# Performance work log

Measured on AMD Instinct MI355X. Metric: run time of the kernel, lower is better.

The kernel has to match this reference:

```python
import jax, jax.numpy as jnp
import numpy as np

B, T, C, H = 16, 2048, 512, 64


def _skew(x):
    # x: (B, T1, T2) -> relative-position skew trick (Music Transformer)
    b, t1, t2 = x.shape
    x = jnp.pad(x, ((0, 0), (0, 0), (1, 0)))        # pad one column on the left
    x = x.reshape(b, t2 + 1, t1)                    # reinterpret layout
    x = x[:, 1:, :]                                 # drop first row
    return jnp.transpose(x, (0, 2, 1))              # (B, T1, T2)


def setup_inputs() -> dict:
    key = jax.random.key(0)
    ks = jax.random.split(key, 5)
    return {
        "x": jax.random.normal(ks[0], (B, T, C), dtype=jnp.float32),
        "Wq": jax.random.normal(ks[1], (C, H), dtype=jnp.float32) * 0.02,
        "Wk": jax.random.normal(ks[2], (C, H), dtype=jnp.float32) * 0.02,
        "Wv": jax.random.normal(ks[3], (C, H), dtype=jnp.float32) * 0.02,
        "Er": jax.random.normal(ks[4], (T, H), dtype=jnp.float32),
    }


def reference(x, Wq, Wk, Wv, Er):
    b, t, c = x.shape
    q = x @ Wq  # (B, T, H)
    k = x @ Wk
    v = x @ Wv
    scale = 1.0 / (k.shape[-1] ** 0.5)
    att = jnp.einsum("bth,bsh->bts", q, k) * scale  # (B, T, T)
    # relative position bias via skew trick
    rel_att = jnp.einsum("bth,rh->btr", q, Er[:t])  # (B, T, T)
    att = att + _skew(rel_att)
    # causal mask
    mask = jnp.tril(jnp.ones((t, t), dtype=bool))
    att = jnp.where(mask, att, -jnp.inf)
    att = jax.nn.softmax(att, axis=-1)
    # dropout is identity in eval mode
    out = att @ v  # (B, T, H)
    return out
```

## Files before the change

kernel.cpp:

```cpp
#include <hip/hip_runtime.h>
#include <hip/hip_bf16.h>

#define TT 2048
#define HB 64
#define NB 16

typedef __attribute__((ext_vector_type(8))) short short8;
typedef __attribute__((ext_vector_type(4))) float floatx4;

static __device__ __forceinline__ unsigned short f2bf(float f) {
  __hip_bfloat16 h = __float2bfloat16(f);
  return *reinterpret_cast<unsigned short*>(&h);
}
static __device__ __forceinline__ float bf2f(unsigned short u) {
  __hip_bfloat16 h = *reinterpret_cast<__hip_bfloat16*>(&u);
  return __bfloat162float(h);
}

__global__ __launch_bounds__(256) void prep_kernel(
    const float* __restrict__ Wq, const float* __restrict__ Wk,
    const float* __restrict__ Wv, const float* __restrict__ Er,
    unsigned short* __restrict__ Wt, unsigned short* __restrict__ Erb) {
  const int bx = blockIdx.x, tid = threadIdx.x;
  if (bx < 512) {
    int idx = bx * 256 + tid;
    Erb[idx] = f2bf(Er[idx]);
  } else {
    int n = bx - 512;
    const float* Ws[3] = {Wq, Wk, Wv};
#pragma unroll
    for (int m = 0; m < 3; m++)
      for (int k = tid; k < 512; k += 256)
        Wt[(size_t)(m * 64 + n) * 512 + k] = f2bf(Ws[m][(size_t)k * 64 + n]);
  }
}

__global__ __launch_bounds__(256) void proj_kernel(
    const float* __restrict__ x, const unsigned short* __restrict__ Wt,
    unsigned short* __restrict__ qb, unsigned short* __restrict__ kb,
    unsigned short* __restrict__ vT) {
  const int tid = threadIdx.x;
  const int w = tid >> 6, l = tid & 63, quad = l >> 4, lm = l & 15;
  const int m0 = blockIdx.x * 64;
  const int row_a = m0 + w * 16 + lm;

  floatx4 acc[12];
#pragma unroll
  for (int i = 0; i < 12; i++) acc[i] = (floatx4){0.f, 0.f, 0.f, 0.f};

  for (int kt = 0; kt < 512; kt += 64) {
    short8 af[2];
#pragma unroll
    for (int kc = 0; kc < 2; kc++) {
      const float* px = &x[(size_t)row_a * 512 + kt + kc * 32 + quad * 8];
      float4 f0 = *(const float4*)px;
      float4 f1 = *(const float4*)(px + 4);
      short8 s;
      s[0] = f2bf(f0.x); s[1] = f2bf(f0.y); s[2] = f2bf(f0.z); s[3] = f2bf(f0.w);
      s[4] = f2bf(f1.x); s[5] = f2bf(f1.y); s[6] = f2bf(f1.z); s[7] = f2bf(f1.w);
      af[kc] = s;
    }
#pragma unroll
    for (int nt = 0; nt < 12; nt++) {
      const unsigned short* pw =
          &Wt[(size_t)((nt >> 2) * 64 + (nt & 3) * 16 + lm) * 512 + kt + quad * 8];
      short8 b0 = *(const short8*)pw;
      short8 b1 = *(const short8*)(pw + 32);
      acc[nt] = __builtin_amdgcn_mfma_f32_16x16x32_bf16(af[0], b0, acc[nt], 0, 0, 0);
      acc[nt] = __builtin_amdgcn_mfma_f32_16x16x32_bf16(af[1], b1, acc[nt], 0, 0, 0);
    }
  }
  const int b = m0 >> 11;
#pragma unroll
  for (int nt = 0; nt < 12; nt++) {
    int col = (nt & 3) * 16 + lm;
#pragma unroll
    for (int rg = 0; rg < 4; rg++) {
      int row = m0 + w * 16 + quad * 4 + rg;
      unsigned short hv = f2bf(acc[nt][rg]);
      if (nt < 4) qb[(size_t)row * 64 + col] = hv;
      else if (nt < 8) kb[(size_t)row * 64 + col] = hv;
      else vT[(size_t)(b * 64 + col) * 2048 + (row & 2047)] = hv;
    }
  }
}

#define SLICE_B 11264

__global__ __launch_bounds__(256) void attn_kernel(
    const unsigned short* __restrict__ qb, const unsigned short* __restrict__ kb,
    const unsigned short* __restrict__ vT, const unsigned short* __restrict__ Erb,
    float* __restrict__ out, float* __restrict__ Op, float* __restrict__ mp,
    float* __restrict__ lp, int nsplit) {
  __shared__ __align__(16) char smem[4 * SLICE_B];

  const int tid = threadIdx.x;
  const int w = tid >> 6;
  if (w >= nsplit) return;
  const int lane = tid & 63;
  const int quad = lane >> 4, lm = lane & 15;

  float* Ds = (float*)(smem + w * SLICE_B);
  unsigned short* Ps = (unsigned short*)(smem + w * SLICE_B + 8448);
  float* dbv = (float*)(smem + w * SLICE_B + 8448 + 2560);

  const int xcd = blockIdx.x & 7;
  const int u = blockIdx.x >> 3;
  const int b = xcd + ((u & 1) << 3);
  const int it = 63 - (u >> 1);
  const int i0 = it * 32;
  const int s = w;

  const size_t qoff = (size_t)b * (2048 * 64);
  const unsigned short* qB = qb + qoff;
  const unsigned short* kB = kb + qoff;
  const unsigned short* vB = vT + qoff;

  short8 qf[2][2];
#pragma unroll
  for (int mt = 0; mt < 2; mt++)
#pragma unroll
    for (int kc = 0; kc < 2; kc++)
      qf[mt][kc] =
          *(const short8*)&qB[(size_t)(i0 + mt * 16 + lm) * 64 + kc * 32 + quad * 8];

  {
    short8 ebf[2];
#pragma unroll
    for (int kc = 0; kc < 2; kc++) {
      short8 z = (short8){0, 0, 0, 0, 0, 0, 0, 0};
      if (lm == 0)
        z = *(const short8*)&Erb[(size_t)2047 * 64 + kc * 32 + quad * 8];
      ebf[kc] = z;
    }
#pragma unroll
    for (int mt = 0; mt < 2; mt++) {
      floatx4 dacc = (floatx4){0.f, 0.f, 0.f, 0.f};
      dacc = __builtin_amdgcn_mfma_f32_16x16x32_bf16(qf[mt][0], ebf[0], dacc, 0, 0, 0);
      dacc = __builtin_amdgcn_mfma_f32_16x16x32_bf16(qf[mt][1], ebf[1], dacc, 0, 0, 0);
      if (lm == 0) {
#pragma unroll
        for (int rg = 0; rg < 4; rg++)
          dbv[mt * 16 + quad * 4 + rg] = dacc[rg];
      }
    }
  }
  __builtin_amdgcn_wave_barrier();

  floatx4 O[2][4];
#pragma unroll
  for (int mt = 0; mt < 2; mt++)
#pragma unroll
    for (int nt = 0; nt < 4; nt++) O[mt][nt] = (floatx4){0.f, 0.f, 0.f, 0.f};
  float m_st[2][4], l_st[2][4];
#pragma unroll
  for (int mt = 0; mt < 2; mt++)
#pragma unroll
    for (int rg = 0; rg < 4; rg++) { m_st[mt][rg] = -1e30f; l_st[mt][rg] = 0.f; }

  for (int jt = s; jt <= it; jt += nsplit) {
    const int j0 = jt * 32;
    const int d = i0 - j0;
    const int e0 = (d - 33 > 0) ? (d - 33) : 0;

    short8 kf[2][2], uf[2][2], ef[4][2], vf[4];
#pragma unroll
    for (int t = 0; t < 2; t++)
#pragma unroll
      for (int kc = 0; kc < 2; kc++)
        kf[t][kc] =
            *(const short8*)&kB[(size_t)(j0 + t * 16 + lm) * 64 + kc * 32 + quad * 8];
#pragma unroll
    for (int ct = 0; ct < 2; ct++)
#pragma unroll
      for (int kc = 0; kc < 2; kc++) {
        int ur = j0 + ct * 16 + lm + 1;
        if (ur > 2047) ur = 2047;
        uf[ct][kc] = *(const short8*)&qB[(size_t)ur * 64 + kc * 32 + quad * 8];
      }
#pragma unroll
    for (int et = 0; et < 4; et++)
#pragma unroll
      for (int kc = 0; kc < 2; kc++)
        ef[et][kc] = *(const short8*)&Erb[(size_t)(e0 + et * 16 + lm) * 64 +
                                          kc * 32 + quad * 8];
#pragma unroll
    for (int nt = 0; nt < 4; nt++)
      vf[nt] = *(const short8*)&vB[(size_t)(nt * 16 + lm) * 2048 + j0 + quad * 8];

    __builtin_amdgcn_wave_barrier();

#pragma unroll
    for (int ct = 0; ct < 2; ct++)
#pragma unroll
      for (int et = 0; et < 4; et++) {
        floatx4 dacc = (floatx4){0.f, 0.f, 0.f, 0.f};
        dacc = __builtin_amdgcn_mfma_f32_16x16x32_bf16(uf[ct][0], ef[et][0], dacc, 0, 0, 0);
        dacc = __builtin_amdgcn_mfma_f32_16x16x32_bf16(uf[ct][1], ef[et][1], dacc, 0, 0, 0);
#pragma unroll
        for (int rg = 0; rg < 4; rg++)
          Ds[(ct * 16 + quad * 4 + rg) * 66 + et * 16 + lm] = dacc[rg];
      }

    floatx4 S[2][2];
#pragma unroll
    for (int mt = 0; mt < 2; mt++)
#pragma unroll
      for (int t = 0; t < 2; t++) {
        floatx4 a = (floatx4){0.f, 0.f, 0.f, 0.f};
        a = __builtin_amdgcn_mfma_f32_16x16x32_bf16(qf[mt][0], kf[t][0], a, 0, 0, 0);
        a = __builtin_amdgcn_mfma_f32_16x16x32_bf16(qf[mt][1], kf[t][1], a, 0, 0, 0);
        S[mt][t] = a;
      }

    __builtin_amdgcn_wave_barrier();
    asm volatile("s_waitcnt lgkmcnt(0)" ::: "memory");
    __builtin_amdgcn_sched_barrier(0);

#pragma unroll
    for (int mt = 0; mt < 2; mt++)
#pragma unroll
      for (int rg = 0; rg < 4; rg++) {
        const int rloc = mt * 16 + quad * 4 + rg;
        const int i = i0 + rloc;
        float sv[2];
#pragma unroll
        for (int t = 0; t < 2; t++) {
          int j = j0 + t * 16 + lm;
          float raw = 0.125f * S[mt][t][rg];
          float val;
          if (j > i) val = -1e30f;
          else if (j == i) val = raw + dbv[rloc];
          else if (j == i - 1) val = raw;
          else val = raw + Ds[(t * 16 + lm) * 66 + (i - j - 2 - e0)];
          sv[t] = val;
        }
        float mx = fmaxf(sv[0], sv[1]);
        mx = fmaxf(mx, __shfl_xor(mx, 1));
        mx = fmaxf(mx, __shfl_xor(mx, 2));
        mx = fmaxf(mx, __shfl_xor(mx, 4));
        mx = fmaxf(mx, __shfl_xor(mx, 8));
        float m_new = fmaxf(m_st[mt][rg], mx);
        float alpha = __expf(m_st[mt][rg] - m_new);
        float p0 = __expf(sv[0] - m_new);
        float p1 = __expf(sv[1] - m_new);
        float ps = p0 + p1;
        ps += __shfl_xor(ps, 1);
        ps += __shfl_xor(ps, 2);
        ps += __shfl_xor(ps, 4);
        ps += __shfl_xor(ps, 8);
        l_st[mt][rg] = l_st[mt][rg] * alpha + ps;
        m_st[mt][rg] = m_new;
#pragma unroll
        for (int nt = 0; nt < 4; nt++) O[mt][nt][rg] *= alpha;
        Ps[rloc * 40 + lm] = f2bf(p0);
        Ps[rloc * 40 + 16 + lm] = f2bf(p1);
      }

    __builtin_amdgcn_wave_barrier();
    asm volatile("s_waitcnt lgkmcnt(0)" ::: "memory");
    __builtin_amdgcn_sched_barrier(0);

#pragma unroll
    for (int mt = 0; mt < 2; mt++) {
      short8 pa = *(const short8*)&Ps[(mt * 16 + lm) * 40 + quad * 8];
#pragma unroll
      for (int nt = 0; nt < 4; nt++)
        O[mt][nt] = __builtin_amdgcn_mfma_f32_16x16x32_bf16(pa, vf[nt], O[mt][nt], 0, 0, 0);
    }
  }

  if (nsplit == 1) {
#pragma unroll
    for (int mt = 0; mt < 2; mt++)
#pragma unroll
      for (int rg = 0; rg < 4; rg++) {
        float inv = 1.f / l_st[mt][rg];
        int row = i0 + mt * 16 + quad * 4 + rg;
#pragma unroll
        for (int nt = 0; nt < 4; nt++)
          out[qoff + (size_t)row * 64 + nt * 16 + lm] = O[mt][nt][rg] * inv;
      }
  } else {
    float* Ops = Op + (size_t)s * (NB * TT * HB);
#pragma unroll
    for (int mt = 0; mt < 2; mt++)
#pragma unroll
      for (int rg = 0; rg < 4; rg++) {
        int row = i0 + mt * 16 + quad * 4 + rg;
#pragma unroll
        for (int nt = 0; nt < 4; nt++)
          Ops[qoff + (size_t)row * 64 + nt * 16 + lm] = O[mt][nt][rg];
        if (lm == 0) {
          int grow = b * 2048 + row;
          mp[s * 32768 + grow] = m_st[mt][rg];
          lp[s * 32768 + grow] = l_st[mt][rg];
        }
      }
  }
}

__global__ __launch_bounds__(256) void combine_kernel(
    const float* __restrict__ Op, const float* __restrict__ mp,
    const float* __restrict__ lp, float* __restrict__ out, int nsplit) {
  int gid = blockIdx.x * 256 + threadIdx.x;
  int row = gid >> 4;
  float m = -1e30f;
  for (int s = 0; s < nsplit; s++) m = fmaxf(m, mp[s * 32768 + row]);
  float den = 0.f;
  float4 r = {0.f, 0.f, 0.f, 0.f};
  for (int s = 0; s < nsplit; s++) {
    float a = __expf(mp[s * 32768 + row] - m);
    den += a * lp[s * 32768 + row];
    float4 o = *(const float4*)&Op[(size_t)s * 2097152 + (size_t)gid * 4];
    r.x += a * o.x;
    r.y += a * o.y;
    r.z += a * o.z;
    r.w += a * o.w;
  }
  float inv = 1.f / den;
  r.x *= inv; r.y *= inv; r.z *= inv; r.w *= inv;
  *(float4*)&out[(size_t)gid * 4] = r;
}

extern "C" void kernel_launch(void* const* d_in, const int* in_sizes, int n_in,
                              void* d_out, int out_size, void* d_ws,
                              size_t ws_size, hipStream_t stream) {
  const float* x = (const float*)d_in[0];
  const float* Wq = (const float*)d_in[1];
  const float* Wk = (const float*)d_in[2];
  const float* Wv = (const float*)d_in[3];
  const float* Er = (const float*)d_in[4];
  float* out = (float*)d_out;

  unsigned short* qb = (unsigned short*)d_ws;
  unsigned short* kb = qb + 2097152;
  unsigned short* vT = kb + 2097152;
  unsigned short* Wt = vT + 2097152;
  unsigned short* Erb = Wt + 98304;
  const size_t base = 13041664ull;
  const size_t need4 = base + 4ull * 8650752ull;
  const size_t need2 = base + 2ull * 8650752ull;
  const int nsplit = (ws_size >= need4) ? 4 : (ws_size >= need2) ? 2 : 1;

  float* Op = (float*)(Erb + 131072);
  float* mp = Op + (size_t)nsplit * 2097152;
  float* lp = mp + (size_t)nsplit * 32768;

  prep_kernel<<<576, 256, 0, stream>>>(Wq, Wk, Wv, Er, Wt, Erb);
  proj_kernel<<<512, 256, 0, stream>>>(x, Wt, qb, kb, vT);
  attn_kernel<<<1024, 256, 0, stream>>>(qb, kb, vT, Erb, out, Op, mp, lp,
                                        nsplit);
  if (nsplit > 1)
    combine_kernel<<<2048, 256, 0, stream>>>(Op, mp, lp, out, nsplit);
}
```

Measured before the change: 253.6 us.

## Fuse split-KV combine into attention kernel, pair causal tiles, skip rescale

The separate combine kernel and its global partial buffers are replaced by an in-block merge of the four waves' partial softmax states through shared memory, with the output written directly. Each block now handles two query tiles (it and 63-it) to balance causal work across 512 blocks. The online softmax skips the max reduction and rescale when every new score stays within a margin of the running max, and the row sum is reduced only once at the end. This removes the global round trip of partial outputs and one kernel launch, at the cost of a block-wide sync per tile and some extra register pressure from launch bounds of 2.

```diff
diff --git a/kernel.cpp b/kernel.cpp
--- a/kernel.cpp
+++ b/kernel.cpp
@@ -4,6 +4,7 @@
 #define TT 2048
 #define HB 64
 #define NB 16
+#define NSPLIT 4
 
 typedef __attribute__((ext_vector_type(8))) short short8;
 typedef __attribute__((ext_vector_type(4))) float floatx4;
@@ -87,16 +88,14 @@
 
 #define SLICE_B 11264
 
-__global__ __launch_bounds__(256) void attn_kernel(
+__global__ __launch_bounds__(256, 2) void attn_kernel(
     const unsigned short* __restrict__ qb, const unsigned short* __restrict__ kb,
     const unsigned short* __restrict__ vT, const unsigned short* __restrict__ Erb,
-    float* __restrict__ out, float* __restrict__ Op, float* __restrict__ mp,
-    float* __restrict__ lp, int nsplit) {
+    float* __restrict__ out) {
   __shared__ __align__(16) char smem[4 * SLICE_B];
 
   const int tid = threadIdx.x;
   const int w = tid >> 6;
-  if (w >= nsplit) return;
   const int lane = tid & 63;
   const int quad = lane >> 4, lm = lane & 15;
 
@@ -105,10 +104,9 @@
   float* dbv = (float*)(smem + w * SLICE_B + 8448 + 2560);
 
   const int xcd = blockIdx.x & 7;
-  const int u = blockIdx.x >> 3;
-  const int b = xcd + ((u & 1) << 3);
-  const int it = 63 - (u >> 1);
-  const int i0 = it * 32;
+  const int slot = blockIdx.x >> 3;
+  const int b = xcd + ((slot & 1) << 3);
+  const int pr = slot >> 1;
   const int s = w;
 
   const size_t qoff = (size_t)b * (2048 * 64);
@@ -116,211 +114,244 @@
   const unsigned short* kB = kb + qoff;
   const unsigned short* vB = vT + qoff;
 
-  short8 qf[2][2];
-#pragma unroll
-  for (int mt = 0; mt < 2; mt++)
-#pragma unroll
-    for (int kc = 0; kc < 2; kc++)
-      qf[mt][kc] =
-          *(const short8*)&qB[(size_t)(i0 + mt * 16 + lm) * 64 + kc * 32 + quad * 8];
-
-  {
-    short8 ebf[2];
-#pragma unroll
-    for (int kc = 0; kc < 2; kc++) {
-      short8 z = (short8){0, 0, 0, 0, 0, 0, 0, 0};
-      if (lm == 0)
-        z = *(const short8*)&Erb[(size_t)2047 * 64 + kc * 32 + quad * 8];
-      ebf[kc] = z;
-    }
-#pragma unroll
-    for (int mt = 0; mt < 2; mt++) {
-      floatx4 dacc = (floatx4){0.f, 0.f, 0.f, 0.f};
-      dacc = __builtin_amdgcn_mfma_f32_16x16x32_bf16(qf[mt][0], ebf[0], dacc, 0, 0, 0);
-      dacc = __builtin_amdgcn_mfma_f32_16x16x32_bf16(qf[mt][1], ebf[1], dacc, 0, 0, 0);
-      if (lm == 0) {
-#pragma unroll
-        for (int rg = 0; rg < 4; rg++)
-          dbv[mt * 16 + quad * 4 + rg] = dacc[rg];
-      }
-    }
+  for (int ph = 0; ph < 2; ph++) {
+    const int it = ph ? (63 - pr) : pr;
+    const int i0 = it * 32;
+
+    short8 qf[2][2];
+#pragma unroll
+    for (int mt = 0; mt < 2; mt++)
+#pragma unroll
+      for (int kc = 0; kc < 2; kc++)
+        qf[mt][kc] =
+            *(const short8*)&qB[(size_t)(i0 + mt * 16 + lm) * 64 + kc * 32 + quad * 8];
+
+    {
+      short8 ebf[2];
+#pragma unroll
+      for (int kc = 0; kc < 2; kc++) {
+        short8 z = (short8){0, 0, 0, 0, 0, 0, 0, 0};
+        if (lm == 0)
+          z = *(const short8*)&Erb[(size_t)2047 * 64 + kc * 32 + quad * 8];
+        ebf[kc] = z;
+      }
+#pragma unroll
+      for (int mt = 0; mt < 2; mt++) {
+        floatx4 dacc = (floatx4){0.f, 0.f, 0.f, 0.f};
+        dacc = __builtin_amdgcn_mfma_f32_16x16x32_bf16(qf[mt][0], ebf[0], dacc, 0, 0, 0);
+        dacc = __builtin_amdgcn_mfma_f32_16x16x32_bf16(qf[mt][1], ebf[1], dacc, 0, 0, 0);
+        if (lm == 0) {
+#pragma unroll
+          for (int rg = 0; rg < 4; rg++)
+            dbv[mt * 16 + quad * 4 + rg] = dacc[rg];
+        }
+      }
+    }
+    __builtin_amdgcn_wave_barrier();
+
+    floatx4 O[2][4];
+#pragma unroll
+    for (int mt = 0; mt < 2; mt++)
+#pragma unroll
+      for (int nt = 0; nt < 4; nt++) O[mt][nt] = (floatx4){0.f, 0.f, 0.f, 0.f};
+    float m_st[2][4], l_st[2][4];
+#pragma unroll
+    for (int mt = 0; mt < 2; mt++)
+#pragma unroll
+      for (int rg = 0; rg < 4; rg++) { m_st[mt][rg] = -1e30f; l_st[mt][rg] = 0.f; }
+
+    for (int jt = s; jt <= it; jt += NSPLIT) {
+      const int j0 = jt * 32;
+      const int d = i0 - j0;
+      const int e0 = (d - 33 > 0) ? (d - 33) : 0;
+
+      short8 kf[2][2], uf[2][2], ef[4][2], vf[4];
+#pragma unroll
+      for (int t = 0; t < 2; t++)
+#pragma unroll
+        for (int kc = 0; kc < 2; kc++)
+          kf[t][kc] =
+              *(const short8*)&kB[(size_t)(j0 + t * 16 + lm) * 64 + kc * 32 + quad * 8];
+#pragma unroll
+      for (int ct = 0; ct < 2; ct++)
+#pragma unroll
+        for (int kc = 0; kc < 2; kc++) {
+          int ur = j0 + ct * 16 + lm + 1;
+          if (ur > 2047) ur = 2047;
+          uf[ct][kc] = *(const short8*)&qB[(size_t)ur * 64 + kc * 32 + quad * 8];
+        }
+#pragma unroll
+      for (int et = 0; et < 4; et++)
+#pragma unroll
+        for (int kc = 0; kc < 2; kc++)
+          ef[et][kc] = *(const short8*)&Erb[(size_t)(e0 + et * 16 + lm) * 64 +
+                                            kc * 32 + quad * 8];
+#pragma unroll
+      for (int nt = 0; nt < 4; nt++)
+        vf[nt] = *(const short8*)&vB[(size_t)(nt * 16 + lm) * 2048 + j0 + quad * 8];
+
+      __builtin_amdgcn_wave_barrier();
+
+#pragma unroll
+      for (int ct = 0; ct < 2; ct++)
+#pragma unroll
+        for (int et = 0; et < 4; et++) {
+          floatx4 dacc = (floatx4){0.f, 0.f, 0.f, 0.f};
+          dacc = __builtin_amdgcn_mfma_f32_16x16x32_bf16(uf[ct][0], ef[et][0], dacc, 0, 0, 0);
+          dacc = __builtin_amdgcn_mfma_f32_16x16x32_bf16(uf[ct][1], ef[et][1], dacc, 0, 0, 0);
+#pragma unroll
+          for (int rg = 0; rg < 4; rg++)
+            Ds[(ct * 16 + quad * 4 + rg) * 66 + et * 16 + lm] = dacc[rg];
+        }
+
+      floatx4 S[2][2];
+#pragma unroll
+      for (int mt = 0; mt < 2; mt++)
+#pragma unroll
+        for (int t = 0; t < 2; t++) {
+          floatx4 a = (floatx4){0.f, 0.f, 0.f, 0.f};
+          a = __builtin_amdgcn_mfma_f32_16x16x32_bf16(qf[mt][0], kf[t][0], a, 0, 0, 0);
+          a = __builtin_amdgcn_mfma_f32_16x16x32_bf16(qf[mt][1], kf[t][1], a, 0, 0, 0);
+          S[mt][t] = a;
+        }
+
+      __builtin_amdgcn_wave_barrier();
+      asm volatile("s_waitcnt lgkmcnt(0)" ::: "memory");
+      __builtin_amdgcn_sched_barrier(0);
+
+      float sv0[8], sv1[8], lmx[8];
+      bool allok = true;
+#pragma unroll
+      for (int mt = 0; mt < 2; mt++)
+#pragma unroll
+        for (int rg = 0; rg < 4; rg++) {
+          const int c = mt * 4 + rg;
+          const int rloc = mt * 16 + quad * 4 + rg;
+          const int i = i0 + rloc;
+          float v0, v1;
+          {
+            int j = j0 + lm;
+            float raw = 0.125f * S[mt][0][rg];
+            if (j > i) v0 = -1e30f;
+            else if (j == i) v0 = raw + dbv[rloc];
+            else if (j == i - 1) v0 = raw;
+            else v0 = raw + Ds[lm * 66 + (i - j - 2 - e0)];
+          }
+          {
+            int j = j0 + 16 + lm;
+            float raw = 0.125f * S[mt][1][rg];
+            if (j > i) v1 = -1e30f;
+            else if (j == i) v1 = raw + dbv[rloc];
+            else if (j == i - 1) v1 = raw;
+            else v1 = raw + Ds[(16 + lm) * 66 + (i - j - 2 - e0)];
+          }
+          sv0[c] = v0; sv1[c] = v1;
+          lmx[c] = fmaxf(v0, v1);
+          allok = allok && (lmx[c] <= m_st[mt][rg] + 8.f);
+        }
+
+      if (__all((int)allok)) {
+#pragma unroll
+        for (int mt = 0; mt < 2; mt++)
+#pragma unroll
+          for (int rg = 0; rg < 4; rg++) {
+            const int c = mt * 4 + rg;
+            const int rloc = mt * 16 + quad * 4 + rg;
+            float p0 = __expf(sv0[c] - m_st[mt][rg]);
+            float p1 = __expf(sv1[c] - m_st[mt][rg]);
+            l_st[mt][rg] += p0 + p1;
+            Ps[rloc * 40 + lm] = f2bf(p0);
+            Ps[rloc * 40 + 16 + lm] = f2bf(p1);
+          }
+      } else {
+#pragma unroll
+        for (int mt = 0; mt < 2; mt++)
+#pragma unroll
+          for (int rg = 0; rg < 4; rg++) {
+            const int c = mt * 4 + rg;
+            const int rloc = mt * 16 + quad * 4 + rg;
+            float mx = lmx[c];
+            mx = fmaxf(mx, __shfl_xor(mx, 1));
+            mx = fmaxf(mx, __shfl_xor(mx, 2));
+            mx = fmaxf(mx, __shfl_xor(mx, 4));
+            mx = fmaxf(mx, __shfl_xor(mx, 8));
+            float m_new = fmaxf(m_st[mt][rg], mx);
+            float alpha = __expf(m_st[mt][rg] - m_new);
+            float p0 = __expf(sv0[c] - m_new);
+            float p1 = __expf(sv1[c] - m_new);
+            l_st[mt][rg] = l_st[mt][rg] * alpha + (p0 + p1);
+            m_st[mt][rg] = m_new;
+#pragma unroll
+            for (int nt = 0; nt < 4; nt++) O[mt][nt][rg] *= alpha;
+            Ps[rloc * 40 + lm] = f2bf(p0);
+            Ps[rloc * 40 + 16 + lm] = f2bf(p1);
+          }
+      }
+
+      __builtin_amdgcn_wave_barrier();
+      asm volatile("s_waitcnt lgkmcnt(0)" ::: "memory");
+      __builtin_amdgcn_sched_barrier(0);
+
+#pragma unroll
+      for (int mt = 0; mt < 2; mt++) {
+        short8 pa = *(const short8*)&Ps[(mt * 16 + lm) * 40 + quad * 8];
+#pragma unroll
+        for (int nt = 0; nt < 4; nt++)
+          O[mt][nt] = __builtin_amdgcn_mfma_f32_16x16x32_bf16(pa, vf[nt], O[mt][nt], 0, 0, 0);
+      }
+    }
+
+    {
+      float* Os = (float*)(smem + w * SLICE_B);
+      float* mlm = (float*)(smem + w * SLICE_B + 8448);
+      float* mll = (float*)(smem + w * SLICE_B + 8448 + 128);
+#pragma unroll
+      for (int mt = 0; mt < 2; mt++)
+#pragma unroll
+        for (int rg = 0; rg < 4; rg++) {
+          float lr = l_st[mt][rg];
+          lr += __shfl_xor(lr, 1);
+          lr += __shfl_xor(lr, 2);
+          lr += __shfl_xor(lr, 4);
+          lr += __shfl_xor(lr, 8);
+          const int rloc = mt * 16 + quad * 4 + rg;
+          if (lm == 0) { mlm[rloc] = m_st[mt][rg]; mll[rloc] = lr; }
+#pragma unroll
+          for (int nt = 0; nt < 4; nt++)
+            Os[rloc * 65 + nt * 16 + lm] = O[mt][nt][rg];
+        }
+    }
+    __syncthreads();
+    {
+      const int row = tid >> 3, c0 = (tid & 7) * 8;
+      float mstar = -1e30f;
+#pragma unroll
+      for (int s2 = 0; s2 < 4; s2++)
+        mstar = fmaxf(mstar, *(const float*)(smem + s2 * SLICE_B + 8448 + row * 4));
+      float den = 0.f;
+      float acc[8];
+#pragma unroll
+      for (int c = 0; c < 8; c++) acc[c] = 0.f;
+#pragma unroll
+      for (int s2 = 0; s2 < 4; s2++) {
+        const char* sl = smem + s2 * SLICE_B;
+        float ms = *(const float*)(sl + 8448 + row * 4);
+        float ls = *(const float*)(sl + 8448 + 128 + row * 4);
+        float a = __expf(ms - mstar);
+        den += a * ls;
+        const float* osp = (const float*)sl + row * 65 + c0;
+#pragma unroll
+        for (int c = 0; c < 8; c++) acc[c] += a * osp[c];
+      }
+      float inv = 1.f / den;
+      float4 r0 = {acc[0] * inv, acc[1] * inv, acc[2] * inv, acc[3] * inv};
+      float4 r1 = {acc[4] * inv, acc[5] * inv, acc[6] * inv, acc[7] * inv};
+      float* po = &out[qoff + (size_t)(i0 + row) * 64 + c0];
+      *(float4*)po = r0;
+      *((float4*)po + 1) = r1;
+    }
+    __syncthreads();
   }
-  __builtin_amdgcn_wave_barrier();
-
-  floatx4 O[2][4];
-#pragma unroll
-  for (int mt = 0; mt < 2; mt++)
-#pragma unroll
-    for (int nt = 0; nt < 4; nt++) O[mt][nt] = (floatx4){0.f, 0.f, 0.f, 0.f};
-  float m_st[2][4], l_st[2][4];
-#pragma unroll
-  for (int mt = 0; mt < 2; mt++)
-#pragma unroll
-    for (int rg = 0; rg < 4; rg++) { m_st[mt][rg] = -1e30f; l_st[mt][rg] = 0.f; }
-
-  for (int jt = s; jt <= it; jt += nsplit) {
-    const int j0 = jt * 32;
-    const int d = i0 - j0;
-    const int e0 = (d - 33 > 0) ? (d - 33) : 0;
-
-    short8 kf[2][2], uf[2][2], ef[4][2], vf[4];
-#pragma unroll
-    for (int t = 0; t < 2; t++)
-#pragma unroll
-      for (int kc = 0; kc < 2; kc++)
-        kf[t][kc] =
-            *(const short8*)&kB[(size_t)(j0 + t * 16 + lm) * 64 + kc * 32 + quad * 8];
-#pragma unroll
-    for (int ct = 0; ct < 2; ct++)
-#pragma unroll
-      for (int kc = 0; kc < 2; kc++) {
-        int ur = j0 + ct * 16 + lm + 1;
-        if (ur > 2047) ur = 2047;
-        uf[ct][kc] = *(const short8*)&qB[(size_t)ur * 64 + kc * 32 + quad * 8];
-      }
-#pragma unroll
-    for (int et = 0; et < 4; et++)
-#pragma unroll
-      for (int kc = 0; kc < 2; kc++)
-        ef[et][kc] = *(const short8*)&Erb[(size_t)(e0 + et * 16 + lm) * 64 +
-                                          kc * 32 + quad * 8];
-#pragma unroll
-    for (int nt = 0; nt < 4; nt++)
-      vf[nt] = *(const short8*)&vB[(size_t)(nt * 16 + lm) * 2048 + j0 + quad * 8];
-
-    __builtin_amdgcn_wave_barrier();
-
-#pragma unroll
-    for (int ct = 0; ct < 2; ct++)
-#pragma unroll
-      for (int et = 0; et < 4; et++) {
-        floatx4 dacc = (floatx4){0.f, 0.f, 0.f, 0.f};
-        dacc = __builtin_amdgcn_mfma_f32_16x16x32_bf16(uf[ct][0], ef[et][0], dacc, 0, 0, 0);
-        dacc = __builtin_amdgcn_mfma_f32_16x16x32_bf16(uf[ct][1], ef[et][1], dacc, 0, 0, 0);
-#pragma unroll
-        for (int rg = 0; rg < 4; rg++)
-          Ds[(ct * 16 + quad * 4 + rg) * 66 + et * 16 + lm] = dacc[rg];
-      }
-
-    floatx4 S[2][2];
-#pragma unroll
-    for (int mt = 0; mt < 2; mt++)
-#pragma unroll
-      for (int t = 0; t < 2; t++) {
-        floatx4 a = (floatx4){0.f, 0.f, 0.f, 0.f};
-        a = __builtin_amdgcn_mfma_f32_16x16x32_bf16(qf[mt][0], kf[t][0], a, 0, 0, 0);
-        a = __builtin_amdgcn_mfma_f32_16x16x32_bf16(qf[mt][1], kf[t][1], a, 0, 0, 0);
-        S[mt][t] = a;
-      }
-
-    __builtin_amdgcn_wave_barrier();
-    asm volatile("s_waitcnt lgkmcnt(0)" ::: "memory");
-    __builtin_amdgcn_sched_barrier(0);
-
-#pragma unroll
-    for (int mt = 0; mt < 2; mt++)
-#pragma unroll
-      for (int rg = 0; rg < 4; rg++) {
-        const int rloc = mt * 16 + quad * 4 + rg;
-        const int i = i0 + rloc;
-        float sv[2];
-#pragma unroll
-        for (int t = 0; t < 2; t++) {
-          int j = j0 + t * 16 + lm;
-          float raw = 0.125f * S[mt][t][rg];
-          float val;
-          if (j > i) val = -1e30f;
-          else if (j == i) val = raw + dbv[rloc];
-          else if (j == i - 1) val = raw;
-          else val = raw + Ds[(t * 16 + lm) * 66 + (i - j - 2 - e0)];
-          sv[t] = val;
-        }
-        float mx = fmaxf(sv[0], sv[1]);
-        mx = fmaxf(mx, __shfl_xor(mx, 1));
-        mx = fmaxf(mx, __shfl_xor(mx, 2));
-        mx = fmaxf(mx, __shfl_xor(mx, 4));
-        mx = fmaxf(mx, __shfl_xor(mx, 8));
-        float m_new = fmaxf(m_st[mt][rg], mx);
-        float alpha = __expf(m_st[mt][rg] - m_new);
-        float p0 = __expf(sv[0] - m_new);
-        float p1 = __expf(sv[1] - m_new);
-        float ps = p0 + p1;
-        ps += __shfl_xor(ps, 1);
-        ps += __shfl_xor(ps, 2);
-        ps += __shfl_xor(ps, 4);
-        ps += __shfl_xor(ps, 8);
-        l_st[mt][rg] = l_st[mt][rg] * alpha + ps;
-        m_st[mt][rg] = m_new;
-#pragma unroll
-        for (int nt = 0; nt < 4; nt++) O[mt][nt][rg] *= alpha;
-        Ps[rloc * 40 + lm] = f2bf(p0);
-        Ps[rloc * 40 + 16 + lm] = f2bf(p1);
-      }
-
-    __builtin_amdgcn_wave_barrier();
-    asm volatile("s_waitcnt lgkmcnt(0)" ::: "memory");
-    __builtin_amdgcn_sched_barrier(0);
-
-#pragma unroll
-    for (int mt = 0; mt < 2; mt++) {
-      short8 pa = *(const short8*)&Ps[(mt * 16 + lm) * 40 + quad * 8];
-#pragma unroll
-      for (int nt = 0; nt < 4; nt++)
-        O[mt][nt] = __builtin_amdgcn_mfma_f32_16x16x32_bf16(pa, vf[nt], O[mt][nt], 0, 0, 0);
-    }
-  }
-
-  if (nsplit == 1) {
-#pragma unroll
-    for (int mt = 0; mt < 2; mt++)
-#pragma unroll
-      for (int rg = 0; rg < 4; rg++) {
-        float inv = 1.f / l_st[mt][rg];
-        int row = i0 + mt * 16 + quad * 4 + rg;
-#pragma unroll
-        for (int nt = 0; nt < 4; nt++)
-          out[qoff + (size_t)row * 64 + nt * 16 + lm] = O[mt][nt][rg] * inv;
-      }
-  } else {
-    float* Ops = Op + (size_t)s * (NB * TT * HB);
-#pragma unroll
-    for (int mt = 0; mt < 2; mt++)
-#pragma unroll
-      for (int rg = 0; rg < 4; rg++) {
-        int row = i0 + mt * 16 + quad * 4 + rg;
-#pragma unroll
-        for (int nt = 0; nt < 4; nt++)
-          Ops[qoff + (size_t)row * 64 + nt * 16 + lm] = O[mt][nt][rg];
-        if (lm == 0) {
-          int grow = b * 2048 + row;
-          mp[s * 32768 + grow] = m_st[mt][rg];
-          lp[s * 32768 + grow] = l_st[mt][rg];
-        }
-      }
-  }
-}
-
-__global__ __launch_bounds__(256) void combine_kernel(
-    const float* __restrict__ Op, const float* __restrict__ mp,
-    const float* __restrict__ lp, float* __restrict__ out, int nsplit) {
-  int gid = blockIdx.x * 256 + threadIdx.x;
-  int row = gid >> 4;
-  float m = -1e30f;
-  for (int s = 0; s < nsplit; s++) m = fmaxf(m, mp[s * 32768 + row]);
-  float den = 0.f;
-  float4 r = {0.f, 0.f, 0.f, 0.f};
-  for (int s = 0; s < nsplit; s++) {
-    float a = __expf(mp[s * 32768 + row] - m);
-    den += a * lp[s * 32768 + row];
-    float4 o = *(const float4*)&Op[(size_t)s * 2097152 + (size_t)gid * 4];
-    r.x += a * o.x;
-    r.y += a * o.y;
-    r.z += a * o.z;
-    r.w += a * o.w;
-  }
-  float inv = 1.f / den;
-  r.x *= inv; r.y *= inv; r.z *= inv; r.w *= inv;
-  *(float4*)&out[(size_t)gid * 4] = r;
 }
 
 extern "C" void kernel_launch(void* const* d_in, const int* in_sizes, int n_in,
@@ -338,19 +369,8 @@
   unsigned short* vT = kb + 2097152;
   unsigned short* Wt = vT + 2097152;
   unsigned short* Erb = Wt + 98304;
-  const size_t base = 13041664ull;
-  const size_t need4 = base + 4ull * 8650752ull;
-  const size_t need2 = base + 2ull * 8650752ull;
-  const int nsplit = (ws_size >= need4) ? 4 : (ws_size >= need2) ? 2 : 1;
-
-  float* Op = (float*)(Erb + 131072);
-  float* mp = Op + (size_t)nsplit * 2097152;
-  float* lp = mp + (size_t)nsplit * 32768;
 
   prep_kernel<<<576, 256, 0, stream>>>(Wq, Wk, Wv, Er, Wt, Erb);
   proj_kernel<<<512, 256, 0, stream>>>(x, Wt, qb, kb, vT);
-  attn_kernel<<<1024, 256, 0, stream>>>(qb, kb, vT, Erb, out, Op, mp, lp,
-                                        nsplit);
-  if (nsplit > 1)
-    combine_kernel<<<2048, 256, 0, stream>>>(Op, mp, lp, out, nsplit);
-}
+  attn_kernel<<<512, 256, 0, stream>>>(qb, kb, vT, Erb, out);
+}
```

Measured after the change: 234.8 us. 1.08x faster.
